# Optimization experiments

Hardware: AMD Instinct MI355X
Metric: run time of the kernel (lower is better)

## Reference

```python
import jax, jax.numpy as jnp
import numpy as np

HID = 2048
HEADS = 16
HD = HID // HEADS  # 128


def setup_inputs() -> dict:
    key = jax.random.key(0)
    ks = jax.random.split(key, 9)
    s = 0.02
    return {
        "hidden_state": jax.random.normal(ks[0], (2, 2048, HID), dtype=jnp.float32),
        "Wq": jax.random.normal(ks[1], (HID, HID), dtype=jnp.float32) * s,
        "bq": jnp.zeros((HID,), dtype=jnp.float32),
        "Wk": jax.random.normal(ks[2], (HID, HD), dtype=jnp.float32) * s,
        "bk": jnp.zeros((HD,), dtype=jnp.float32),
        "Wv": jax.random.normal(ks[3], (HID, HD), dtype=jnp.float32) * s,
        "bv": jnp.zeros((HD,), dtype=jnp.float32),
        "Wo": jax.random.normal(ks[4], (HID, HID), dtype=jnp.float32) * s,
        "bo": jnp.zeros((HID,), dtype=jnp.float32),
    }


def reference(hidden_state, Wq, bq, Wk, bk, Wv, bv, Wo, bo):
    bs, seq, _ = hidden_state.shape
    # Q: [b, s, H, hd] -> per-head; K,V: single shared head [b, s, hd]
    q = (hidden_state @ Wq + bq).reshape(bs, seq, HEADS, HD)
    k = hidden_state @ Wk + bk  # [b, s, hd]
    v = hidden_state @ Wv + bv  # [b, s, hd]
    scale = 1.0 / jnp.sqrt(jnp.float32(HD))
    # scores: [b, h, s_q, s_k] against shared K head
    scores = jnp.einsum("bqhd,bkd->bhqk", q, k) * scale
    attn = jax.nn.softmax(scores, axis=-1)
    out = jnp.einsum("bhqk,bkd->bqhd", attn, v)  # [b, s, h, hd]
    out = out.reshape(bs, seq, HID)
    return out @ Wo + bo
```

## Files before the change

### kernel.cpp

```cpp
#include <hip/hip_runtime.h>
#include <math.h>

#define HIDN 2048
#define NHEADS 16
#define HDIM 128
#define SEQ 2048
#define NB 2

#define C2 0.12751744154f

typedef __bf16 bf16x8 __attribute__((ext_vector_type(8)));
typedef float f32x4 __attribute__((ext_vector_type(4)));

__device__ __forceinline__ unsigned short f32_to_bf16(float f) {
  unsigned int u = __float_as_uint(f);
  u += 0x7FFFu + ((u >> 16) & 1u);
  return (unsigned short)(u >> 16);
}

__device__ __forceinline__ unsigned pack_bf16x2(float a, float b) {
  return (unsigned)f32_to_bf16(a) | ((unsigned)f32_to_bf16(b) << 16);
}

__device__ __forceinline__ unsigned pack_bf16x2_trunc(float a, float b) {
  return __builtin_amdgcn_perm(__float_as_uint(b), __float_as_uint(a), 0x07060302u);
}

__device__ __forceinline__ void gload_lds16(const void* g, void* l) {
  __builtin_amdgcn_global_load_lds(
      (__attribute__((address_space(1))) void*)(g),
      (__attribute__((address_space(3))) void*)(l), 16, 0, 0);
}

__global__ __launch_bounds__(256) void cast_f32_bf16(
    const float* __restrict__ in, unsigned short* __restrict__ out, int n4) {
  int i = blockIdx.x * blockDim.x + threadIdx.x;
  if (i >= n4) return;
  float4 v = ((const float4*)in)[i];
  ushort4 o;
  o.x = f32_to_bf16(v.x); o.y = f32_to_bf16(v.y);
  o.z = f32_to_bf16(v.z); o.w = f32_to_bf16(v.w);
  ((ushort4*)out)[i] = o;
}

__global__ __launch_bounds__(256) void wtrans_big(
    const float* __restrict__ wq, unsigned short* __restrict__ dq,
    const float* __restrict__ wo, unsigned short* __restrict__ do_) {
  __shared__ float tile[32][33];
  const float* src = blockIdx.z ? wo : wq;
  unsigned short* dst = blockIdx.z ? do_ : dq;
  const float m = blockIdx.z ? 1.0f : C2;
  int c0 = blockIdx.x * 32, r0 = blockIdx.y * 32;
  int tx = threadIdx.x & 31, ty = threadIdx.x >> 5;
#pragma unroll
  for (int i = 0; i < 32; i += 8)
    tile[ty + i][tx] = src[(size_t)(r0 + ty + i) * 2048 + c0 + tx];
  __syncthreads();
#pragma unroll
  for (int i = 0; i < 32; i += 8)
    dst[(size_t)(c0 + ty + i) * 2048 + r0 + tx] = f32_to_bf16(tile[tx][ty + i] * m);
}

__global__ __launch_bounds__(256) void wtrans_small(
    const float* __restrict__ wk, const float* __restrict__ wv,
    unsigned short* __restrict__ dk, unsigned short* __restrict__ dv,
    const float* __restrict__ bq, const float* __restrict__ bk,
    const float* __restrict__ bv, float* __restrict__ biasout) {
  __shared__ float tile[32][33];
  const float* src = blockIdx.z ? wv : wk;
  unsigned short* dst = blockIdx.z ? dv : dk;
  int c0 = blockIdx.x * 32, r0 = blockIdx.y * 32;
  int tx = threadIdx.x & 31, ty = threadIdx.x >> 5;
#pragma unroll
  for (int i = 0; i < 32; i += 8)
    tile[ty + i][tx] = src[(size_t)(r0 + ty + i) * 128 + c0 + tx];
  __syncthreads();
#pragma unroll
  for (int i = 0; i < 32; i += 8)
    dst[(size_t)(c0 + ty + i) * 2048 + r0 + tx] = f32_to_bf16(tile[tx][ty + i]);
  if (blockIdx.z == 0) {
    int lb = blockIdx.y * 4 + blockIdx.x;
    if (lb < 9) {
      int i = lb * 256 + threadIdx.x;
      if (i < 2304)
        biasout[i] = (i < 2048) ? bq[i] * C2
                                : ((i < 2176) ? bk[i - 2048] : bv[i - 2176]);
    }
  }
}

__global__ __launch_bounds__(256) void vtrans(
    const unsigned short* __restrict__ qkv, unsigned short* __restrict__ vt) {
  __shared__ unsigned short tile[32][33];
  const unsigned short* src = qkv + (size_t)blockIdx.z * SEQ * 2304 + 2176;
  unsigned short* dst = vt + (size_t)blockIdx.z * 128 * SEQ;
  int c0 = blockIdx.x * 32, r0 = blockIdx.y * 32;
  int tx = threadIdx.x & 31, ty = threadIdx.x >> 5;
#pragma unroll
  for (int i = 0; i < 32; i += 8)
    tile[ty + i][tx] = src[(size_t)(r0 + ty + i) * 2304 + c0 + tx];
  __syncthreads();
  const int s = r0 + tx;
  const int col = (s & ~63) | (((s >> 5) & 1) * 32 + ((s >> 2) & 3) * 8 +
                               ((s >> 4) & 1) * 4 + (s & 3));
#pragma unroll
  for (int i = 0; i < 32; i += 8)
    dst[(size_t)(c0 + ty + i) * SEQ + col] = tile[tx][ty + i];
}

template <int BN>
__global__ __launch_bounds__(256) void gemm_bt(
    const unsigned short* __restrict__ A,
    const unsigned short* __restrict__ BT,
    const float* __restrict__ bias,
    void* __restrict__ C, int K, int ldc, int outBf16) {
  constexpr int NT = BN / 32;
  __shared__ unsigned short As[128 * 64];
  __shared__ unsigned short Bs[BN * 64];
  const int tid = threadIdx.x;
  const int lane = tid & 63;
  const int wave = tid >> 6;
  const int wr = wave >> 1, wc = wave & 1;
  const int ml = lane & 15, quad = lane >> 4;
  const long bm = (long)blockIdx.x * 128;
  const long bn = (long)blockIdx.y * BN;

  const f32x4 zero4 = {0.f, 0.f, 0.f, 0.f};
  f32x4 acc[4][NT];
#pragma unroll
  for (int mt = 0; mt < 4; ++mt)
#pragma unroll
    for (int nt = 0; nt < NT; ++nt) acc[mt][nt] = zero4;

  const int srow = lane >> 3;
  const int scol = ((lane & 7) ^ srow) * 8;

  for (int k0 = 0; k0 < K; k0 += 64) {
    __syncthreads();
#pragma unroll
    for (int r = 0; r < 4; ++r) {
      const int rowb = r * 32 + wave * 8;
      gload_lds16(A + (bm + rowb + srow) * (long)K + k0 + scol, &As[rowb * 64]);
    }
#pragma unroll
    for (int r = 0; r < NT; ++r) {
      const int rowb = r * 32 + wave * 8;
      gload_lds16(BT + (bn + rowb + srow) * (long)K + k0 + scol, &Bs[rowb * 64]);
    }
    __syncthreads();
#pragma unroll
    for (int kk = 0; kk < 64; kk += 32) {
      const int g0 = (kk >> 3) + quad;
      bf16x8 af[4], bf[NT];
#pragma unroll
      for (int mt = 0; mt < 4; ++mt)
        af[mt] = *(const bf16x8*)&As[(wr * 64 + mt * 16 + ml) * 64 +
                                     ((g0 ^ (ml & 7)) << 3)];
#pragma unroll
      for (int nt = 0; nt < NT; ++nt)
        bf[nt] = *(const bf16x8*)&Bs[(wc * (BN / 2) + nt * 16 + ml) * 64 +
                                     ((g0 ^ (ml & 7)) << 3)];
#pragma unroll
      for (int mt = 0; mt < 4; ++mt)
#pragma unroll
        for (int nt = 0; nt < NT; ++nt)
          acc[mt][nt] = __builtin_amdgcn_mfma_f32_16x16x32_bf16(
              af[mt], bf[nt], acc[mt][nt], 0, 0, 0);
    }
  }

#pragma unroll
  for (int mt = 0; mt < 4; ++mt) {
#pragma unroll
    for (int nt = 0; nt < NT; ++nt) {
      const long col = bn + wc * (BN / 2) + nt * 16 + ml;
      const float bval = bias ? bias[col] : 0.f;
#pragma unroll
      for (int r = 0; r < 4; ++r) {
        const long row = bm + wr * 64 + mt * 16 + quad * 4 + r;
        const float v = acc[mt][nt][r] + bval;
        if (outBf16)
          ((unsigned short*)C)[row * ldc + col] = f32_to_bf16(v);
        else
          ((float*)C)[row * ldc + col] = v;
      }
    }
  }
}

__global__ __launch_bounds__(256, 2) void mqa_attn(
    const unsigned short* __restrict__ qkv,
    const unsigned short* __restrict__ vt,
    unsigned short* __restrict__ outp) {
  __shared__ unsigned short Ks[2][64 * 128];
  __shared__ unsigned short VTs[2][128 * 64];

  const int lane = threadIdx.x & 63;
  const int wave = threadIdx.x >> 6;
  const int ml = lane & 15, quad = lane >> 4;
  const int h = blockIdx.y, b = blockIdx.z;
  const long q0 = (long)blockIdx.x * 128;
  const long base = (long)b * SEQ;

  bf16x8 aq[2][4];
#pragma unroll
  for (int n = 0; n < 2; ++n) {
    const unsigned short* qrow =
        qkv + (base + q0 + wave * 32 + n * 16 + ml) * 2304 + h * 128;
#pragma unroll
    for (int ks = 0; ks < 4; ++ks)
      aq[n][ks] = *(const bf16x8*)(qrow + ks * 32 + quad * 8);
  }

  const f32x4 zero4 = {0.f, 0.f, 0.f, 0.f};
  f32x4 o[8][2];
#pragma unroll
  for (int mt2 = 0; mt2 < 8; ++mt2)
#pragma unroll
    for (int n = 0; n < 2; ++n) o[mt2][n] = zero4;
  f32x4 o9[2] = {zero4, zero4};

  bf16x8 ones_af;
  {
    union { unsigned u[4]; bf16x8 v; } cv;
    const unsigned w = (ml == 0) ? 0x3F803F80u : 0u;
    cv.u[0] = w; cv.u[1] = w; cv.u[2] = w; cv.u[3] = w;
    ones_af = cv.v;
  }

  const int srowK = lane >> 4;
  const int scolK = ((lane & 15) ^ (wave * 4 + srowK)) * 8;
  const int srowV = lane >> 3;
  const int scolV = ((lane & 7) ^ srowV) * 8;
  const unsigned short* kp = qkv + (base + srowK) * 2304 + 2048 + scolK;
  const unsigned short* vp = vt + ((long)b * 128 + srowV) * SEQ + scolV;

  auto stage = [&](int buf, int ktn) {
    const unsigned short* kpp = kp + (long)ktn * (64 * 2304);
    const unsigned short* vpp = vp + ktn * 64;
#pragma unroll
    for (int r = 0; r < 4; ++r) {
      const int rowb = r * 16 + wave * 4;
      gload_lds16(kpp + (long)rowb * 2304, &Ks[buf][rowb * 128]);
    }
#pragma unroll
    for (int r = 0; r < 4; ++r) {
      const int rowb = r * 32 + wave * 8;
      gload_lds16(vpp + (long)rowb * SEQ, &VTs[buf][rowb * 64]);
    }
  };

  stage(0, 0);

  for (int kt = 0; kt < SEQ / 64; ++kt) {
    const int cur = kt & 1;
    __syncthreads();
    if (kt < SEQ / 64 - 1) stage(cur ^ 1, kt + 1);

    f32x4 s[4][2];
#pragma unroll
    for (int mt = 0; mt < 4; ++mt)
#pragma unroll
      for (int n = 0; n < 2; ++n) s[mt][n] = zero4;
#pragma unroll
    for (int ks = 0; ks < 4; ++ks) {
#pragma unroll
      for (int mt = 0; mt < 4; ++mt) {
        bf16x8 ak = *(const bf16x8*)&Ks[cur][(mt * 16 + ml) * 128 +
                                            (((ks * 4 + quad) ^ ml) << 3)];
#pragma unroll
        for (int n = 0; n < 2; ++n)
          s[mt][n] = __builtin_amdgcn_mfma_f32_16x16x32_bf16(
              ak, aq[n][ks], s[mt][n], 0, 0, 0);
      }
    }

    unsigned pk[2][4][2];
#pragma unroll
    for (int mt = 0; mt < 4; ++mt)
#pragma unroll
      for (int n = 0; n < 2; ++n) {
        const float p0 = __builtin_amdgcn_exp2f(s[mt][n][0]);
        const float p1 = __builtin_amdgcn_exp2f(s[mt][n][1]);
        const float p2 = __builtin_amdgcn_exp2f(s[mt][n][2]);
        const float p3 = __builtin_amdgcn_exp2f(s[mt][n][3]);
        pk[n][mt][0] = pack_bf16x2_trunc(p0, p1);
        pk[n][mt][1] = pack_bf16x2_trunc(p2, p3);
      }

#pragma unroll
    for (int ks2 = 0; ks2 < 2; ++ks2) {
      bf16x8 bp[2];
#pragma unroll
      for (int n = 0; n < 2; ++n) {
        union { unsigned u[4]; bf16x8 v; } cv;
        cv.u[0] = pk[n][2 * ks2][0];
        cv.u[1] = pk[n][2 * ks2][1];
        cv.u[2] = pk[n][2 * ks2 + 1][0];
        cv.u[3] = pk[n][2 * ks2 + 1][1];
        bp[n] = cv.v;
      }
#pragma unroll
      for (int n = 0; n < 2; ++n)
        o9[n] = __builtin_amdgcn_mfma_f32_16x16x32_bf16(
            ones_af, bp[n], o9[n], 0, 0, 0);
#pragma unroll
      for (int mt2 = 0; mt2 < 8; ++mt2) {
        bf16x8 av = *(const bf16x8*)&VTs[cur][(mt2 * 16 + ml) * 64 +
                                             (((ks2 * 4 + quad) ^ (ml & 7)) << 3)];
#pragma unroll
        for (int n = 0; n < 2; ++n)
          o[mt2][n] = __builtin_amdgcn_mfma_f32_16x16x32_bf16(
              av, bp[n], o[mt2][n], 0, 0, 0);
      }
    }
  }

  float inv[2];
#pragma unroll
  for (int n = 0; n < 2; ++n)
    inv[n] = 1.f / __shfl(o9[n][0], ml);

#pragma unroll
  for (int n = 0; n < 2; ++n) {
    const long row = base + q0 + wave * 32 + n * 16 + ml;
#pragma unroll
    for (int mt2 = 0; mt2 < 8; ++mt2) {
      uint2 w;
      w.x = pack_bf16x2(o[mt2][n][0] * inv[n], o[mt2][n][1] * inv[n]);
      w.y = pack_bf16x2(o[mt2][n][2] * inv[n], o[mt2][n][3] * inv[n]);
      *(uint2*)&outp[row * HIDN + h * HDIM + mt2 * 16 + quad * 4] = w;
    }
  }
}

extern "C" void kernel_launch(void* const* d_in, const int* in_sizes, int n_in,
                              void* d_out, int out_size, void* d_ws, size_t ws_size,
                              hipStream_t stream) {
  const float* hidden = (const float*)d_in[0];
  const float* Wq = (const float*)d_in[1];
  const float* bq = (const float*)d_in[2];
  const float* Wk = (const float*)d_in[3];
  const float* bk = (const float*)d_in[4];
  const float* Wv = (const float*)d_in[5];
  const float* bv = (const float*)d_in[6];
  const float* Wo = (const float*)d_in[7];
  const float* bo = (const float*)d_in[8];
  float* out = (float*)d_out;

  char* ws = (char*)d_ws;
  const size_t MB = 1u << 20;
  unsigned short* hb    = (unsigned short*)(ws);
  unsigned short* attn  = hb;
  unsigned short* wqkvT = (unsigned short*)(ws + 16 * MB);
  unsigned short* woT   = (unsigned short*)(ws + 25 * MB);
  unsigned short* qkv   = (unsigned short*)(ws + 33 * MB);
  unsigned short* vt    = (unsigned short*)(ws + 51 * MB);
  float* biasqkv        = (float*)(ws + 52 * MB);

  cast_f32_bf16<<<8192, 256, 0, stream>>>(hidden, hb, (NB * SEQ * HIDN) / 4);
  wtrans_big<<<dim3(64, 64, 2), 256, 0, stream>>>(Wq, wqkvT, Wo, woT);
  wtrans_small<<<dim3(4, 64, 2), 256, 0, stream>>>(
      Wk, Wv, wqkvT + (size_t)2048 * 2048, wqkvT + (size_t)2176 * 2048,
      bq, bk, bv, biasqkv);

  gemm_bt<96><<<dim3(32, 24), 256, 0, stream>>>(hb, wqkvT, biasqkv, qkv, 2048, 2304, 1);

  vtrans<<<dim3(4, 64, 2), 256, 0, stream>>>(qkv, vt);

  mqa_attn<<<dim3(SEQ / 128, NHEADS, NB), 256, 0, stream>>>(qkv, vt, attn);

  gemm_bt<128><<<dim3(32, 16), 256, 0, stream>>>(attn, woT, bo, out, 2048, 2048, 0);
}
```

Before: 280.4 us.

## Merge prep kernels, fuse V transpose into QKV GEMM, split attention barriers

Three prep kernels (input cast and the two weight-transpose passes) are merged into one launch. The QKV GEMM epilogue now writes the permuted V-transpose layout directly, which removes the separate vtrans kernel. In the attention loop, the full __syncthreads is replaced with partial vmcnt waits plus raw barriers so the K tile can be consumed before the V loads finish. This cuts launch overhead and one pass over V, at the cost of scattered 8-byte stores in the GEMM epilogue and fragile hand-counted waitcnt values.

```diff
diff --git a/kernel.cpp b/kernel.cpp
--- a/kernel.cpp
+++ b/kernel.cpp
@@ -32,88 +32,76 @@
       (__attribute__((address_space(3))) void*)(l), 16, 0, 0);
 }
 
-__global__ __launch_bounds__(256) void cast_f32_bf16(
-    const float* __restrict__ in, unsigned short* __restrict__ out, int n4) {
-  int i = blockIdx.x * blockDim.x + threadIdx.x;
-  if (i >= n4) return;
-  float4 v = ((const float4*)in)[i];
-  ushort4 o;
-  o.x = f32_to_bf16(v.x); o.y = f32_to_bf16(v.y);
-  o.z = f32_to_bf16(v.z); o.w = f32_to_bf16(v.w);
-  ((ushort4*)out)[i] = o;
-}
-
-__global__ __launch_bounds__(256) void wtrans_big(
+__global__ __launch_bounds__(256) void prep(
+    const float* __restrict__ hidden, unsigned short* __restrict__ hb,
     const float* __restrict__ wq, unsigned short* __restrict__ dq,
-    const float* __restrict__ wo, unsigned short* __restrict__ do_) {
-  __shared__ float tile[32][33];
-  const float* src = blockIdx.z ? wo : wq;
-  unsigned short* dst = blockIdx.z ? do_ : dq;
-  const float m = blockIdx.z ? 1.0f : C2;
-  int c0 = blockIdx.x * 32, r0 = blockIdx.y * 32;
-  int tx = threadIdx.x & 31, ty = threadIdx.x >> 5;
-#pragma unroll
-  for (int i = 0; i < 32; i += 8)
-    tile[ty + i][tx] = src[(size_t)(r0 + ty + i) * 2048 + c0 + tx];
-  __syncthreads();
-#pragma unroll
-  for (int i = 0; i < 32; i += 8)
-    dst[(size_t)(c0 + ty + i) * 2048 + r0 + tx] = f32_to_bf16(tile[tx][ty + i] * m);
-}
-
-__global__ __launch_bounds__(256) void wtrans_small(
+    const float* __restrict__ wo, unsigned short* __restrict__ do_,
     const float* __restrict__ wk, const float* __restrict__ wv,
     unsigned short* __restrict__ dk, unsigned short* __restrict__ dv,
     const float* __restrict__ bq, const float* __restrict__ bk,
     const float* __restrict__ bv, float* __restrict__ biasout) {
   __shared__ float tile[32][33];
-  const float* src = blockIdx.z ? wv : wk;
-  unsigned short* dst = blockIdx.z ? dv : dk;
-  int c0 = blockIdx.x * 32, r0 = blockIdx.y * 32;
-  int tx = threadIdx.x & 31, ty = threadIdx.x >> 5;
-#pragma unroll
-  for (int i = 0; i < 32; i += 8)
-    tile[ty + i][tx] = src[(size_t)(r0 + ty + i) * 128 + c0 + tx];
-  __syncthreads();
-#pragma unroll
-  for (int i = 0; i < 32; i += 8)
-    dst[(size_t)(c0 + ty + i) * 2048 + r0 + tx] = f32_to_bf16(tile[tx][ty + i]);
-  if (blockIdx.z == 0) {
-    int lb = blockIdx.y * 4 + blockIdx.x;
-    if (lb < 9) {
-      int i = lb * 256 + threadIdx.x;
-      if (i < 2304)
-        biasout[i] = (i < 2048) ? bq[i] * C2
-                                : ((i < 2176) ? bk[i - 2048] : bv[i - 2176]);
-    }
-  }
-}
-
-__global__ __launch_bounds__(256) void vtrans(
-    const unsigned short* __restrict__ qkv, unsigned short* __restrict__ vt) {
-  __shared__ unsigned short tile[32][33];
-  const unsigned short* src = qkv + (size_t)blockIdx.z * SEQ * 2304 + 2176;
-  unsigned short* dst = vt + (size_t)blockIdx.z * 128 * SEQ;
-  int c0 = blockIdx.x * 32, r0 = blockIdx.y * 32;
-  int tx = threadIdx.x & 31, ty = threadIdx.x >> 5;
-#pragma unroll
-  for (int i = 0; i < 32; i += 8)
-    tile[ty + i][tx] = src[(size_t)(r0 + ty + i) * 2304 + c0 + tx];
-  __syncthreads();
-  const int s = r0 + tx;
-  const int col = (s & ~63) | (((s >> 5) & 1) * 32 + ((s >> 2) & 3) * 8 +
-                               ((s >> 4) & 1) * 4 + (s & 3));
-#pragma unroll
-  for (int i = 0; i < 32; i += 8)
-    dst[(size_t)(c0 + ty + i) * SEQ + col] = tile[tx][ty + i];
-}
-
-template <int BN>
+  const int blk = blockIdx.x;
+  const int tx = threadIdx.x & 31, ty = threadIdx.x >> 5;
+  if (blk < 8192) {
+    int i = blk * 256 + threadIdx.x;
+    float4 v = ((const float4*)hidden)[i];
+    ushort4 o;
+    o.x = f32_to_bf16(v.x); o.y = f32_to_bf16(v.y);
+    o.z = f32_to_bf16(v.z); o.w = f32_to_bf16(v.w);
+    ((ushort4*)hb)[i] = o;
+    return;
+  }
+  if (blk < 16384) {
+    int r = blk - 8192;
+    const int z = r >> 12; r &= 4095;
+    const int bx = r & 63, by = r >> 6;
+    const float* src = z ? wo : wq;
+    unsigned short* dst = z ? do_ : dq;
+    const float m = z ? 1.0f : C2;
+    const int c0 = bx * 32, r0 = by * 32;
+#pragma unroll
+    for (int i = 0; i < 32; i += 8)
+      tile[ty + i][tx] = src[(size_t)(r0 + ty + i) * 2048 + c0 + tx];
+    __syncthreads();
+#pragma unroll
+    for (int i = 0; i < 32; i += 8)
+      dst[(size_t)(c0 + ty + i) * 2048 + r0 + tx] = f32_to_bf16(tile[tx][ty + i] * m);
+    return;
+  }
+  {
+    int r = blk - 16384;
+    const int z = r >> 8; r &= 255;
+    const int bx = r & 3, by = r >> 2;
+    const float* src = z ? wv : wk;
+    unsigned short* dst = z ? dv : dk;
+    const int c0 = bx * 32, r0 = by * 32;
+#pragma unroll
+    for (int i = 0; i < 32; i += 8)
+      tile[ty + i][tx] = src[(size_t)(r0 + ty + i) * 128 + c0 + tx];
+    __syncthreads();
+#pragma unroll
+    for (int i = 0; i < 32; i += 8)
+      dst[(size_t)(c0 + ty + i) * 2048 + r0 + tx] = f32_to_bf16(tile[tx][ty + i]);
+    if (z == 0) {
+      int lb = by * 4 + bx;
+      if (lb < 9) {
+        int i = lb * 256 + threadIdx.x;
+        if (i < 2304)
+          biasout[i] = (i < 2048) ? bq[i] * C2
+                                  : ((i < 2176) ? bk[i - 2048] : bv[i - 2176]);
+      }
+    }
+  }
+}
+
+template <int BN, int WRITE_VT>
 __global__ __launch_bounds__(256) void gemm_bt(
     const unsigned short* __restrict__ A,
     const unsigned short* __restrict__ BT,
     const float* __restrict__ bias,
-    void* __restrict__ C, int K, int ldc, int outBf16) {
+    void* __restrict__ C, unsigned short* __restrict__ vtout,
+    int K, int ldc, int outBf16) {
   constexpr int NT = BN / 32;
   __shared__ unsigned short As[128 * 64];
   __shared__ unsigned short Bs[BN * 64];
@@ -175,14 +163,30 @@
     for (int nt = 0; nt < NT; ++nt) {
       const long col = bn + wc * (BN / 2) + nt * 16 + ml;
       const float bval = bias ? bias[col] : 0.f;
+      float vv[4];
 #pragma unroll
       for (int r = 0; r < 4; ++r) {
         const long row = bm + wr * 64 + mt * 16 + quad * 4 + r;
         const float v = acc[mt][nt][r] + bval;
+        vv[r] = v;
         if (outBf16)
           ((unsigned short*)C)[row * ldc + col] = f32_to_bf16(v);
         else
           ((float*)C)[row * ldc + col] = v;
+      }
+      if (WRITE_VT) {
+        if (col >= 2176) {
+          const long row0 = bm + wr * 64 + mt * 16 + quad * 4;
+          const int b = (int)(row0 >> 11);
+          const int s0 = (int)(row0 & 2047);
+          const int P = (s0 & ~63) | (((s0 >> 5) & 1) * 32 +
+                                      (((s0 >> 2) & 3) * 8) +
+                                      (((s0 >> 4) & 1) * 4));
+          uint2 w;
+          w.x = pack_bf16x2(vv[0], vv[1]);
+          w.y = pack_bf16x2(vv[2], vv[3]);
+          *(uint2*)&vtout[((long)b * 128 + (col - 2176)) * SEQ + P] = w;
+        }
       }
     }
   }
@@ -254,7 +258,8 @@
 
   for (int kt = 0; kt < SEQ / 64; ++kt) {
     const int cur = kt & 1;
-    __syncthreads();
+    asm volatile("s_waitcnt vmcnt(4)" ::: "memory");
+    __builtin_amdgcn_s_barrier();
     if (kt < SEQ / 64 - 1) stage(cur ^ 1, kt + 1);
 
     f32x4 s[4][2];
@@ -287,6 +292,12 @@
         pk[n][mt][0] = pack_bf16x2_trunc(p0, p1);
         pk[n][mt][1] = pack_bf16x2_trunc(p2, p3);
       }
+
+    if (kt < SEQ / 64 - 1)
+      asm volatile("s_waitcnt vmcnt(8)" ::: "memory");
+    else
+      asm volatile("s_waitcnt vmcnt(0)" ::: "memory");
+    __builtin_amdgcn_s_barrier();
 
 #pragma unroll
     for (int ks2 = 0; ks2 < 2; ++ks2) {
@@ -358,17 +369,16 @@
   unsigned short* vt    = (unsigned short*)(ws + 51 * MB);
   float* biasqkv        = (float*)(ws + 52 * MB);
 
-  cast_f32_bf16<<<8192, 256, 0, stream>>>(hidden, hb, (NB * SEQ * HIDN) / 4);
-  wtrans_big<<<dim3(64, 64, 2), 256, 0, stream>>>(Wq, wqkvT, Wo, woT);
-  wtrans_small<<<dim3(4, 64, 2), 256, 0, stream>>>(
-      Wk, Wv, wqkvT + (size_t)2048 * 2048, wqkvT + (size_t)2176 * 2048,
-      bq, bk, bv, biasqkv);
-
-  gemm_bt<96><<<dim3(32, 24), 256, 0, stream>>>(hb, wqkvT, biasqkv, qkv, 2048, 2304, 1);
-
-  vtrans<<<dim3(4, 64, 2), 256, 0, stream>>>(qkv, vt);
+  prep<<<16896, 256, 0, stream>>>(hidden, hb, Wq, wqkvT, Wo, woT, Wk, Wv,
+                                  wqkvT + (size_t)2048 * 2048,
+                                  wqkvT + (size_t)2176 * 2048,
+                                  bq, bk, bv, biasqkv);
+
+  gemm_bt<96, 1><<<dim3(32, 24), 256, 0, stream>>>(
+      hb, wqkvT, biasqkv, qkv, vt, 2048, 2304, 1);
 
   mqa_attn<<<dim3(SEQ / 128, NHEADS, NB), 256, 0, stream>>>(qkv, vt, attn);
 
-  gemm_bt<128><<<dim3(32, 16), 256, 0, stream>>>(attn, woT, bo, out, 2048, 2048, 0);
-}
+  gemm_bt<128, 0><<<dim3(32, 16), 256, 0, stream>>>(
+      attn, woT, bo, out, nullptr, 2048, 2048, 0);
+}
```

New measurement: 276.2 us. No clear change (-1.5%).
